# Kernel tuning notes

Hardware: AMD Instinct MI355X
Metric: run time of the kernel (lower is better)

Reference implementation:

```python
import jax, jax.numpy as jnp
import numpy as np

N_LAYERS = 2
D_CONV = 4
D_MODEL = 768
D_INNER = 1536
D_STATE = 16
D_DELTA = 48
B = 2
L = 1024
EPS = 1e-5


def setup_inputs() -> dict:
    key = jax.random.key(0)
    ks = jax.random.split(key, 8)
    s = 0.02
    x = jax.random.normal(ks[0], (B, L, D_MODEL), jnp.float32)
    in_proj_w = jax.random.normal(ks[1], (N_LAYERS, 2 * D_INNER, D_MODEL), jnp.float32) * s
    conv_w = jax.random.normal(ks[2], (N_LAYERS, D_INNER, 1, D_CONV), jnp.float32) * s
    conv_b = jnp.zeros((N_LAYERS, D_INNER), jnp.float32)
    xproj_w = jax.random.normal(ks[3], (N_LAYERS, D_DELTA + 2 * D_STATE, D_INNER), jnp.float32) * s
    dt_w = jax.random.normal(ks[4], (N_LAYERS, D_INNER, D_DELTA), jnp.float32) * s
    dt_b = jax.random.normal(ks[5], (N_LAYERS, D_INNER), jnp.float32) * s
    A_log = jnp.tile(jnp.log(jnp.arange(1, D_STATE + 1, dtype=jnp.float32)), (N_LAYERS, D_INNER, 1))
    D = jnp.ones((N_LAYERS, D_INNER), jnp.float32)
    out_proj_w = jax.random.normal(ks[6], (N_LAYERS, D_MODEL, D_INNER), jnp.float32) * s
    norm_w = jnp.ones((N_LAYERS, D_MODEL), jnp.float32)
    return dict(x=x, in_proj_w=in_proj_w, conv_w=conv_w, conv_b=conv_b,
                xproj_w=xproj_w, dt_w=dt_w, dt_b=dt_b, A_log=A_log, D=D,
                out_proj_w=out_proj_w, norm_w=norm_w)


def rms_norm(x, w):
    return w * x * jax.lax.rsqrt(jnp.mean(x * x, axis=-1, keepdims=True) + EPS)


def causal_depthwise_conv(x, w, b):
    # x: [B, L, D_INNER], w: [D_INNER, 1, K], b: [D_INNER]
    xc = x.transpose(0, 2, 1)  # [B, D, L]
    y = jax.lax.conv_general_dilated(
        xc, w, window_strides=(1,), padding=[(D_CONV - 1, 0)],
        dimension_numbers=("NCH", "OIH", "NCH"), feature_group_count=D_INNER)
    y = y + b[None, :, None]
    return y.transpose(0, 2, 1)  # [B, L, D]


def ssm(x, A_log, D, xproj_w, dt_w, dt_b):
    # x: [B, L, D_INNER]
    A = -jnp.exp(A_log)  # [D, N]
    dbc = jnp.einsum('bld,ed->ble', x, xproj_w)
    delta, Bc, C = jnp.split(dbc, [D_DELTA, D_DELTA + D_STATE], axis=-1)
    delta = jax.nn.softplus(jnp.einsum('blr,dr->bld', delta, dt_w) + dt_b)  # [B, L, D]
    dA = jnp.exp(delta[..., None] * A)                          # [B, L, D, N]
    dBx = delta[..., None] * Bc[:, :, None, :] * x[..., None]   # [B, L, D, N]

    def step(h, inp):
        dA_t, dBx_t, C_t = inp
        h = dA_t * h + dBx_t                      # [B, D, N]
        y = jnp.einsum('bdn,bn->bd', h, C_t)      # [B, D]
        return h, y

    h0 = jnp.zeros((x.shape[0], D_INNER, D_STATE), x.dtype)
    _, ys = jax.lax.scan(step, h0, (dA.transpose(1, 0, 2, 3),
                                    dBx.transpose(1, 0, 2, 3),
                                    C.transpose(1, 0, 2)))
    y = ys.transpose(1, 0, 2)  # [B, L, D]
    return y + D * x


def mamba_block(x, in_w, cw, cb, xp_w, dtw, dtb, Alog, Dp, out_w):
    xz = jnp.einsum('blm,em->ble', x, in_w)           # [B, L, 2*D_INNER]
    xi, z = jnp.split(xz, 2, axis=-1)
    xi = jax.nn.silu(causal_depthwise_conv(xi, cw, cb))
    y = ssm(xi, Alog, Dp, xp_w, dtw, dtb)
    out = y * jax.nn.silu(z)
    return jnp.einsum('bld,md->blm', out, out_w)


def reference(x, in_proj_w, conv_w, conv_b, xproj_w, dt_w, dt_b, A_log, D, out_proj_w, norm_w):
    for i in range(N_LAYERS):
        x = x + mamba_block(rms_norm(x, norm_w[i]), in_proj_w[i], conv_w[i], conv_b[i],
                            xproj_w[i], dt_w[i], dt_b[i], A_log[i], D[i], out_proj_w[i])
    return x
```

## Files before the change

### kernel.cpp

```cpp
#include <hip/hip_runtime.h>
#include <hip/hip_bf16.h>
#include <cstdint>

#define NL 2
#define DM 768
#define DI 1536
#define DS 16
#define DD 48
#define DCONV 4
#define BB 2
#define LL 1024
#define MROWS (BB*LL)
#define DBCW (DD + 2*DS)
#define TC 32
#define NC (LL/TC)
#define KSPL 4
#define XPN 128

typedef __bf16 bf16x8 __attribute__((ext_vector_type(8)));
typedef float f32x4 __attribute__((ext_vector_type(4)));
using bf16 = __hip_bfloat16;

__device__ __forceinline__ float softplusf(float x) {
  return (x > 20.f) ? x : log1pf(__expf(x));
}

__device__ __forceinline__ void load_lds16(const void* g, void* l) {
  __builtin_amdgcn_global_load_lds(
      (const __attribute__((address_space(1))) void*)g,
      (__attribute__((address_space(3))) void*)l, 16, 0, 0);
}

#define WI_N (NL*2*DI*DM)
#define WX_N (NL*XPN*DI)
#define WD_N (NL*DI*DD)
#define WO_N (NL*DM*DI)
__global__ __launch_bounds__(256)
void prep_weights(const float* __restrict__ wi, const float* __restrict__ wx,
                  const float* __restrict__ wd, const float* __restrict__ wo,
                  bf16* __restrict__ bi, bf16* __restrict__ bx,
                  bf16* __restrict__ bd, bf16* __restrict__ bo)
{
  int i = blockIdx.x * 256 + threadIdx.x;
  if (i < WI_N) { bi[i] = __float2bfloat16(wi[i]); return; }
  i -= WI_N;
  if (i < WX_N) {
    const int l = i / (XPN*DI), r = (i / DI) % XPN, k = i % DI;
    const float v = (r < DBCW) ? wx[((size_t)l*DBCW + r)*DI + k] : 0.f;
    bx[i] = __float2bfloat16(v); return;
  }
  i -= WX_N;
  if (i < WD_N) { bd[i] = __float2bfloat16(wd[i]); return; }
  i -= WD_N;
  if (i < WO_N) { bo[i] = __float2bfloat16(wo[i]); }
}

__global__ __launch_bounds__(256)
void rmsnorm_kernel(const float* __restrict__ x, const float* __restrict__ w,
                    bf16* __restrict__ out)
{
  const int row = blockIdx.x;
  const float* xr = x + (size_t)row * DM;
  const int t = threadIdx.x;
  float v0 = xr[t], v1 = xr[t + 256], v2 = xr[t + 512];
  float ss = v0*v0 + v1*v1 + v2*v2;
  #pragma unroll
  for (int off = 32; off > 0; off >>= 1) ss += __shfl_down(ss, off);
  __shared__ float sred[4];
  if ((t & 63) == 0) sred[t >> 6] = ss;
  __syncthreads();
  const float scale = rsqrtf((sred[0]+sred[1]+sred[2]+sred[3]) * (1.f/DM) + 1e-5f);
  out[(size_t)row*DM + t      ] = __float2bfloat16(v0 * scale * w[t]);
  out[(size_t)row*DM + t + 256] = __float2bfloat16(v1 * scale * w[t + 256]);
  out[(size_t)row*DM + t + 512] = __float2bfloat16(v2 * scale * w[t + 512]);
}

__global__ __launch_bounds__(256)
void gemm_in128(const bf16* __restrict__ A, const bf16* __restrict__ W,
                float* __restrict__ xzf, bf16* __restrict__ zb)
{
  __shared__ __align__(16) bf16 As[128][32];
  __shared__ __align__(16) bf16 Ws[128][32];
  const int tid = threadIdx.x;
  const int wave = tid >> 6, lane = tid & 63;
  const int m0 = blockIdx.x * 128, n0 = blockIdx.y * 128;
  const int wr = (wave >> 1) * 64, wc = (wave & 1) * 64;
  const int l16 = lane & 15, quad = lane >> 4;
  const int srow = wave * 16 + (lane >> 2);
  const int scol = (lane & 3) * 8;
  bf16* a_base0 = &As[wave*16][0];
  bf16* a_base1 = &As[64 + wave*16][0];
  bf16* w_base0 = &Ws[wave*16][0];
  bf16* w_base1 = &Ws[64 + wave*16][0];

  f32x4 acc[4][4] = {};

  for (int k0 = 0; k0 < DM; k0 += 32) {
    load_lds16(A + (size_t)(m0 + srow) * DM + k0 + scol,      a_base0);
    load_lds16(A + (size_t)(m0 + 64 + srow) * DM + k0 + scol, a_base1);
    load_lds16(W + (size_t)(n0 + srow) * DM + k0 + scol,      w_base0);
    load_lds16(W + (size_t)(n0 + 64 + srow) * DM + k0 + scol, w_base1);
    __syncthreads();

    bf16x8 af[4], wf[4];
    #pragma unroll
    for (int i = 0; i < 4; ++i)
      af[i] = *reinterpret_cast<const bf16x8*>(&As[wr + i*16 + l16][quad*8]);
    #pragma unroll
    for (int j = 0; j < 4; ++j)
      wf[j] = *reinterpret_cast<const bf16x8*>(&Ws[wc + j*16 + l16][quad*8]);
    #pragma unroll
    for (int i = 0; i < 4; ++i)
      #pragma unroll
      for (int j = 0; j < 4; ++j)
        acc[i][j] = __builtin_amdgcn_mfma_f32_16x16x32_bf16(af[i], wf[j], acc[i][j], 0, 0, 0);
    __syncthreads();
  }

  const bool isz = (n0 >= DI);
  #pragma unroll
  for (int i = 0; i < 4; ++i) {
    #pragma unroll
    for (int j = 0; j < 4; ++j) {
      const int col = n0 + wc + j*16 + l16;
      #pragma unroll
      for (int r = 0; r < 4; ++r) {
        const int row = m0 + wr + i*16 + quad*4 + r;
        const float v = acc[i][j][r];
        if (!isz) xzf[(size_t)row*DI + col] = v;
        else      zb[(size_t)row*DI + col - DI] = __float2bfloat16(v);
      }
    }
  }
}

template<int MODE>
__global__ __launch_bounds__(256)
void gemm64l(const bf16* __restrict__ A, int lda,
             const bf16* __restrict__ W, int ldw,
             float* __restrict__ C, int ldc, int N, int K,
             const float* __restrict__ res)
{
  __shared__ __align__(16) bf16 As[64][32];
  __shared__ __align__(16) bf16 Ws[64][32];
  const int tid = threadIdx.x;
  const int wave = tid >> 6, lane = tid & 63;
  const int m0 = blockIdx.x * 64, n0 = blockIdx.y * 64;
  const int wr = (wave >> 1) * 32, wc = (wave & 1) * 32;
  const int l16 = lane & 15, quad = lane >> 4;
  const int srow = wave * 16 + (lane >> 2);
  const int scol = (lane & 3) * 8;
  bf16* a_base = &As[wave*16][0];
  bf16* w_base = &Ws[wave*16][0];

  A += (size_t)blockIdx.z * K;
  W += (size_t)blockIdx.z * K;
  C += (size_t)blockIdx.z * MROWS * ldc;

  f32x4 acc[2][2] = {};

  for (int k0 = 0; k0 < K; k0 += 32) {
    load_lds16(A + (size_t)(m0 + srow) * lda + k0 + scol, a_base);
    load_lds16(W + (size_t)(n0 + srow) * ldw + k0 + scol, w_base);
    __syncthreads();
    bf16x8 af[2], wf[2];
    #pragma unroll
    for (int i = 0; i < 2; ++i)
      af[i] = *reinterpret_cast<const bf16x8*>(&As[wr + i*16 + l16][quad*8]);
    #pragma unroll
    for (int j = 0; j < 2; ++j)
      wf[j] = *reinterpret_cast<const bf16x8*>(&Ws[wc + j*16 + l16][quad*8]);
    #pragma unroll
    for (int i = 0; i < 2; ++i)
      #pragma unroll
      for (int j = 0; j < 2; ++j)
        acc[i][j] = __builtin_amdgcn_mfma_f32_16x16x32_bf16(af[i], wf[j], acc[i][j], 0, 0, 0);
    __syncthreads();
  }

  #pragma unroll
  for (int i = 0; i < 2; ++i) {
    #pragma unroll
    for (int j = 0; j < 2; ++j) {
      const int col = n0 + wc + j*16 + l16;
      if (col >= N) continue;
      #pragma unroll
      for (int r = 0; r < 4; ++r) {
        const int row = m0 + wr + i*16 + quad*4 + r;
        float v = acc[i][j][r];
        const size_t idx = (size_t)row * ldc + col;
        if (MODE == 3) v += res[idx];
        C[idx] = v;
      }
    }
  }
}

__global__ __launch_bounds__(256)
void xproj_reduce(const float* __restrict__ part, bf16* __restrict__ dbcb,
                  float* __restrict__ bcf)
{
  const int idx = blockIdx.x * 256 + threadIdx.x;
  const int row = idx / DBCW, col = idx % DBCW;
  float v = part[idx];
  #pragma unroll
  for (int z = 1; z < KSPL; ++z) v += part[idx + (size_t)z*MROWS*DBCW];
  if (col < DD) dbcb[(size_t)row*DD + col] = __float2bfloat16(v);
  else          bcf[(size_t)row*32 + col - DD] = v;
}

__global__ __launch_bounds__(256)
void conv_silu_kernel(const float* __restrict__ xzf, const float* __restrict__ cw,
                      const float* __restrict__ cb, bf16* __restrict__ xob)
{
  const int idx = blockIdx.x * 256 + threadIdx.x;
  const int d = idx % DI;
  const int row = idx / DI;
  const int l = row % LL;
  float acc = cb[d];
  #pragma unroll
  for (int k = 0; k < DCONV; ++k) {
    const int ll = l - (DCONV-1) + k;
    if (ll >= 0)
      acc += cw[d*DCONV + k] * xzf[(size_t)(row - (DCONV-1) + k) * DI + d];
  }
  const float s = acc / (1.f + __expf(-acc));
  xob[idx] = __float2bfloat16(s);
}

__global__ __launch_bounds__(256)
void gemm_dt(const bf16* __restrict__ A, const bf16* __restrict__ W,
             bf16* __restrict__ Cb, const float* __restrict__ bias)
{
  __shared__ __align__(16) bf16 As[64][40];
  __shared__ __align__(16) bf16 Ws[64][40];
  const int tid = threadIdx.x;
  const int m0 = blockIdx.x * 64, n0 = blockIdx.y * 64;
  const int wave = tid >> 6, lane = tid & 63;
  const int wr = (wave >> 1) * 32, wc = (wave & 1) * 32;
  const int l16 = lane & 15, quad = lane >> 4;
  const int srow = tid >> 2;
  const int scol = (tid & 3) * 8;

  f32x4 acc[2][2] = {};

  #pragma unroll
  for (int k0 = 0; k0 < DD; k0 += 32) {
    {
      const bf16* src = A + (size_t)(m0 + srow) * DD + (k0 + scol);
      bf16* dst = &As[srow][scol];
      if (k0 + scol + 8 <= DD) {
        *reinterpret_cast<uint4*>(dst) = *reinterpret_cast<const uint4*>(src);
      } else {
        #pragma unroll
        for (int j = 0; j < 8; ++j)
          dst[j] = (k0 + scol + j < DD) ? src[j] : __float2bfloat16(0.f);
      }
    }
    {
      const bf16* src = W + (size_t)(n0 + srow) * DD + (k0 + scol);
      bf16* dst = &Ws[srow][scol];
      if (k0 + scol + 8 <= DD) {
        *reinterpret_cast<uint4*>(dst) = *reinterpret_cast<const uint4*>(src);
      } else {
        #pragma unroll
        for (int j = 0; j < 8; ++j)
          dst[j] = (k0 + scol + j < DD) ? src[j] : __float2bfloat16(0.f);
      }
    }
    __syncthreads();
    bf16x8 af[2], wf[2];
    #pragma unroll
    for (int i = 0; i < 2; ++i)
      af[i] = *reinterpret_cast<const bf16x8*>(&As[wr + i*16 + l16][quad*8]);
    #pragma unroll
    for (int j = 0; j < 2; ++j)
      wf[j] = *reinterpret_cast<const bf16x8*>(&Ws[wc + j*16 + l16][quad*8]);
    #pragma unroll
    for (int i = 0; i < 2; ++i)
      #pragma unroll
      for (int j = 0; j < 2; ++j)
        acc[i][j] = __builtin_amdgcn_mfma_f32_16x16x32_bf16(af[i], wf[j], acc[i][j], 0, 0, 0);
    __syncthreads();
  }

  #pragma unroll
  for (int i = 0; i < 2; ++i) {
    #pragma unroll
    for (int j = 0; j < 2; ++j) {
      const int col = n0 + wc + j*16 + l16;
      #pragma unroll
      for (int r = 0; r < 4; ++r) {
        const int row = m0 + wr + i*16 + quad*4 + r;
        Cb[(size_t)row*DI + col] = __float2bfloat16(softplusf(acc[i][j][r] + bias[col]));
      }
    }
  }
}

__global__ __launch_bounds__(256)
void scan_pass1(const bf16* __restrict__ delta, const bf16* __restrict__ xi,
                const float* __restrict__ bcf, const float* __restrict__ A_log,
                float* __restrict__ P, float* __restrict__ H)
{
  __shared__ float Bs[TC][DS];
  const int tid = threadIdx.x;
  const int wave = tid >> 6, lane = tid & 63;
  const int s = lane >> 5;
  const int dloc = wave*32 + (lane & 31);
  const int dt = blockIdx.x % (DI/128);
  const int c  = (blockIdx.x / (DI/128)) % NC;
  const int b  =  blockIdx.x / ((DI/128)*NC);
  const int d  = dt*128 + dloc;
  const int t0 = c*TC;

  {
    const int t = tid >> 4, n = tid & 15;
    Bs[t][n]      = bcf[((size_t)b*LL + t0 + t)*32 + n];
    Bs[t + 16][n] = bcf[((size_t)b*LL + t0 + 16 + t)*32 + n];
  }
  float An[8];
  {
    const float4* ap = (const float4*)(A_log + (size_t)d*DS + s*8);
    float4 v0 = ap[0], v1 = ap[1];
    An[0] = -__expf(v0.x)*1.44269504f; An[1] = -__expf(v0.y)*1.44269504f;
    An[2] = -__expf(v0.z)*1.44269504f; An[3] = -__expf(v0.w)*1.44269504f;
    An[4] = -__expf(v1.x)*1.44269504f; An[5] = -__expf(v1.y)*1.44269504f;
    An[6] = -__expf(v1.z)*1.44269504f; An[7] = -__expf(v1.w)*1.44269504f;
  }
  __syncthreads();

  const bf16* dptr = delta + ((size_t)b*LL + t0)*DI + d;
  const bf16* xptr = xi    + ((size_t)b*LL + t0)*DI + d;
  float h[8] = {0.f,0.f,0.f,0.f,0.f,0.f,0.f,0.f};
  float sdl = 0.f;
  #pragma unroll
  for (int t = 0; t < TC; ++t) {
    const float dl = __bfloat162float(dptr[(size_t)t*DI]);
    const float xv = __bfloat162float(xptr[(size_t)t*DI]);
    const float dlxv = dl * xv;
    sdl += dl;
    const float4* brow = (const float4*)&Bs[t][s*8];
    const float4 b0 = brow[0], b1 = brow[1];
    const float bb[8] = {b0.x,b0.y,b0.z,b0.w,b1.x,b1.y,b1.z,b1.w};
    #pragma unroll
    for (int n = 0; n < 8; ++n) {
      const float dA = exp2f(dl * An[n]);
      h[n] = dA*h[n] + dlxv*bb[n];
    }
  }
  const size_t base = (((size_t)b*NC + c)*DI + d)*DS + s*8;
  float4* Pp = (float4*)(P + base);
  float4* Hp = (float4*)(H + base);
  Pp[0] = make_float4(exp2f(An[0]*sdl), exp2f(An[1]*sdl), exp2f(An[2]*sdl), exp2f(An[3]*sdl));
  Pp[1] = make_float4(exp2f(An[4]*sdl), exp2f(An[5]*sdl), exp2f(An[6]*sdl), exp2f(An[7]*sdl));
  Hp[0] = make_float4(h[0],h[1],h[2],h[3]);
  Hp[1] = make_float4(h[4],h[5],h[6],h[7]);
}

__global__ __launch_bounds__(256)
void scan_fix(const float* __restrict__ P, float* __restrict__ H)
{
  const int idx = blockIdx.x * 256 + threadIdx.x;
  const int n = idx & 15;
  const int d = (idx >> 4) % DI;
  const int b = idx / (DS * DI);
  float hin = 0.f;
  #pragma unroll 8
  for (int c = 0; c < NC; ++c) {
    const size_t ic = (((size_t)b*NC + c)*DI + d)*DS + n;
    const float Pv = P[ic];
    const float Hv = H[ic];
    H[ic] = hin;
    hin = fmaf(Pv, hin, Hv);
  }
}

__global__ __launch_bounds__(256)
void scan_pass2(const bf16* __restrict__ delta, const bf16* __restrict__ xi,
                const float* __restrict__ bcf, const float* __restrict__ A_log,
                const float* __restrict__ H, const float* __restrict__ Dp,
                const bf16* __restrict__ zb, bf16* __restrict__ outb)
{
  __shared__ float Bs[TC][DS];
  __shared__ float Cs[TC][DS];
  const int tid = threadIdx.x;
  const int wave = tid >> 6, lane = tid & 63;
  const int s = lane >> 5;
  const int dloc = wave*32 + (lane & 31);
  const int dt = blockIdx.x % (DI/128);
  const int c  = (blockIdx.x / (DI/128)) % NC;
  const int b  =  blockIdx.x / ((DI/128)*NC);
  const int d  = dt*128 + dloc;
  const int t0 = c*TC;

  {
    const int t = tid >> 4, n = tid & 15;
    const size_t r0 = ((size_t)b*LL + t0 + t)*32;
    const size_t r1 = ((size_t)b*LL + t0 + 16 + t)*32;
    Bs[t][n]      = bcf[r0 + n];
    Bs[t + 16][n] = bcf[r1 + n];
    Cs[t][n]      = bcf[r0 + 16 + n];
    Cs[t + 16][n] = bcf[r1 + 16 + n];
  }
  float An[8];
  {
    const float4* ap = (const float4*)(A_log + (size_t)d*DS + s*8);
    float4 v0 = ap[0], v1 = ap[1];
    An[0] = -__expf(v0.x)*1.44269504f; An[1] = -__expf(v0.y)*1.44269504f;
    An[2] = -__expf(v0.z)*1.44269504f; An[3] = -__expf(v0.w)*1.44269504f;
    An[4] = -__expf(v1.x)*1.44269504f; An[5] = -__expf(v1.y)*1.44269504f;
    An[6] = -__expf(v1.z)*1.44269504f; An[7] = -__expf(v1.w)*1.44269504f;
  }
  const float Dd = Dp[d];
  float h[8];
  {
    const float4* hp = (const float4*)(H + (((size_t)b*NC + c)*DI + d)*DS + s*8);
    float4 h0 = hp[0], h1 = hp[1];
    h[0]=h0.x; h[1]=h0.y; h[2]=h0.z; h[3]=h0.w;
    h[4]=h1.x; h[5]=h1.y; h[6]=h1.z; h[7]=h1.w;
  }
  __syncthreads();

  const bf16* dptr = delta + ((size_t)b*LL + t0)*DI + d;
  const bf16* xptr = xi    + ((size_t)b*LL + t0)*DI + d;
  const bf16* zptr = zb    + ((size_t)b*LL + t0)*DI + d;
  bf16* optr = outb + ((size_t)b*LL + t0)*DI + d;

  #pragma unroll
  for (int t = 0; t < TC; ++t) {
    const float dl = __bfloat162float(dptr[(size_t)t*DI]);
    const float xv = __bfloat162float(xptr[(size_t)t*DI]);
    const float zv = __bfloat162float(zptr[(size_t)t*DI]);
    const float dlxv = dl * xv;
    const float4* brow = (const float4*)&Bs[t][s*8];
    const float4* crow = (const float4*)&Cs[t][s*8];
    const float4 b0 = brow[0], b1 = brow[1];
    const float4 c0 = crow[0], c1 = crow[1];
    const float bb[8] = {b0.x,b0.y,b0.z,b0.w,b1.x,b1.y,b1.z,b1.w};
    const float cc[8] = {c0.x,c0.y,c0.z,c0.w,c1.x,c1.y,c1.z,c1.w};
    float y = 0.f;
    #pragma unroll
    for (int n = 0; n < 8; ++n) {
      const float dA = exp2f(dl * An[n]);
      h[n] = dA*h[n] + dlxv*bb[n];
      y = fmaf(h[n], cc[n], y);
    }
    y += __shfl_xor(y, 32);
    if (s == 0) {
      const float o = (y + Dd * xv) * (zv / (1.f + __expf(-zv)));
      optr[(size_t)t*DI] = __float2bfloat16(o);
    }
  }
}

extern "C" void kernel_launch(void* const* d_in, const int* in_sizes, int n_in,
                              void* d_out, int out_size, void* d_ws, size_t ws_size,
                              hipStream_t stream)
{
  const float* x_in   = (const float*)d_in[0];
  const float* w_inp  = (const float*)d_in[1];
  const float* w_conv = (const float*)d_in[2];
  const float* b_conv = (const float*)d_in[3];
  const float* w_xprj = (const float*)d_in[4];
  const float* w_dtp  = (const float*)d_in[5];
  const float* b_dt   = (const float*)d_in[6];
  const float* a_log  = (const float*)d_in[7];
  const float* d_par  = (const float*)d_in[8];
  const float* w_outp = (const float*)d_in[9];
  const float* w_norm = (const float*)d_in[10];
  float* xfinal = (float*)d_out;

  char* ws = (char*)d_ws;
  size_t off = 0;
  auto alloc = [&](size_t bytes) -> void* {
    void* p = ws + off;
    off += (bytes + 255) & ~(size_t)255;
    return p;
  };
  bf16*  wb_in  = (bf16*) alloc((size_t)WI_N*2);
  bf16*  wb_xp  = (bf16*) alloc((size_t)WX_N*2);
  bf16*  wb_dt  = (bf16*) alloc((size_t)WD_N*2);
  bf16*  wb_out = (bf16*) alloc((size_t)WO_N*2);
  bf16*  xn     = (bf16*) alloc((size_t)MROWS*DM*2);
  float* xzf    = (float*)alloc((size_t)MROWS*DI*4);
  bf16*  zb     = (bf16*) alloc((size_t)MROWS*DI*2);
  bf16*  xcb    = (bf16*) alloc((size_t)MROWS*DI*2);
  float* xpart  = (float*)alloc((size_t)KSPL*MROWS*DBCW*4);
  bf16*  dbcb   = (bf16*) alloc((size_t)MROWS*DD*2);
  float* bcf    = (float*)alloc((size_t)MROWS*32*4);
  bf16*  dltb   = (bf16*) alloc((size_t)MROWS*DI*2);
  bf16*  scb    = (bf16*) alloc((size_t)MROWS*DI*2);
  float* x1     = (float*)alloc((size_t)MROWS*DM*4);
  float* Pws    = (float*)alloc((size_t)BB*NC*DI*DS*4);
  float* Hws    = (float*)alloc((size_t)BB*NC*DI*DS*4);

  prep_weights<<<(WI_N+WX_N+WD_N+WO_N + 255)/256, 256, 0, stream>>>(
      w_inp, w_xprj, w_dtp, w_outp, wb_in, wb_xp, wb_dt, wb_out);

  const float* xprev = x_in;
  for (int l = 0; l < NL; ++l) {
    rmsnorm_kernel<<<MROWS, 256, 0, stream>>>(xprev, w_norm + l*DM, xn);

    gemm_in128<<<dim3(MROWS/128, (2*DI)/128), 256, 0, stream>>>(
        xn, wb_in + (size_t)l*2*DI*DM, xzf, zb);

    conv_silu_kernel<<<(MROWS*DI)/256, 256, 0, stream>>>(
        xzf, w_conv + l*DI*DCONV, b_conv + l*DI, xcb);

    gemm64l<0><<<dim3(MROWS/64, XPN/64, KSPL), 256, 0, stream>>>(
        xcb, DI, wb_xp + (size_t)l*XPN*DI, DI, xpart, DBCW, DBCW, DI/KSPL, nullptr);

    xproj_reduce<<<(MROWS*DBCW)/256, 256, 0, stream>>>(xpart, dbcb, bcf);

    gemm_dt<<<dim3(MROWS/64, DI/64), 256, 0, stream>>>(
        dbcb, wb_dt + (size_t)l*DI*DD, dltb, b_dt + l*DI);

    scan_pass1<<<BB*NC*(DI/128), 256, 0, stream>>>(
        dltb, xcb, bcf, a_log + (size_t)l*DI*DS, Pws, Hws);
    scan_fix<<<(BB*DI*DS)/256, 256, 0, stream>>>(Pws, Hws);
    scan_pass2<<<BB*NC*(DI/128), 256, 0, stream>>>(
        dltb, xcb, bcf, a_log + (size_t)l*DI*DS, Hws, d_par + l*DI, zb, scb);

    float* xout = (l == NL-1) ? xfinal : x1;
    gemm64l<3><<<dim3(MROWS/64, DM/64, 1), 256, 0, stream>>>(
        scb, DI, wb_out + (size_t)l*DM*DI, DI, xout, DM, DM, DI, xprev);

    xprev = x1;
  }
}
```

Baseline: 392.7 us.

## Fuse scan passes with grid barriers, fold reductions into consumers, split-K out-proj

The three scan kernels become one persistent kernel that uses global atomic grid barriers between the chunk pass, the prefix fix-up and the output pass. The x-projection split-K reduction moves into the dt GEMM's load path, and the in-projection now writes the x half as bf16 instead of fp32. The out-projection uses a 128-tile split-K GEMM whose partial sums are reduced in a new kernel that also adds the residual and applies the next layer's RMSNorm. Together these cut launches and intermediate traffic, but the grid barrier relies on all 768 scan blocks being resident at once, which risks deadlock if occupancy falls short.

```diff
diff --git a/kernel.cpp b/kernel.cpp
--- a/kernel.cpp
+++ b/kernel.cpp
@@ -16,6 +16,7 @@
 #define NC (LL/TC)
 #define KSPL 4
 #define XPN 128
+#define SCAN_BLOCKS (BB*NC*(DI/128))
 
 typedef __bf16 bf16x8 __attribute__((ext_vector_type(8)));
 typedef float f32x4 __attribute__((ext_vector_type(4)));
@@ -31,6 +32,18 @@
       (__attribute__((address_space(3))) void*)l, 16, 0, 0);
 }
 
+__device__ __forceinline__ void grid_barrier(unsigned* slot, unsigned nb) {
+  __syncthreads();
+  if (threadIdx.x == 0) {
+    __threadfence();
+    __hip_atomic_fetch_add(slot, 1u, __ATOMIC_RELEASE, __HIP_MEMORY_SCOPE_AGENT);
+    while (__hip_atomic_load(slot, __ATOMIC_ACQUIRE, __HIP_MEMORY_SCOPE_AGENT) < nb)
+      __builtin_amdgcn_s_sleep(2);
+    __threadfence();
+  }
+  __syncthreads();
+}
+
 #define WI_N (NL*2*DI*DM)
 #define WX_N (NL*XPN*DI)
 #define WD_N (NL*DI*DD)
@@ -39,8 +52,10 @@
 void prep_weights(const float* __restrict__ wi, const float* __restrict__ wx,
                   const float* __restrict__ wd, const float* __restrict__ wo,
                   bf16* __restrict__ bi, bf16* __restrict__ bx,
-                  bf16* __restrict__ bd, bf16* __restrict__ bo)
-{
+                  bf16* __restrict__ bd, bf16* __restrict__ bo,
+                  unsigned* __restrict__ bar)
+{
+  if (blockIdx.x == 0 && threadIdx.x < 8) bar[threadIdx.x] = 0u;
   int i = blockIdx.x * 256 + threadIdx.x;
   if (i < WI_N) { bi[i] = __float2bfloat16(wi[i]); return; }
   i -= WI_N;
@@ -75,9 +90,12 @@
   out[(size_t)row*DM + t + 512] = __float2bfloat16(v2 * scale * w[t + 512]);
 }
 
-__global__ __launch_bounds__(256)
-void gemm_in128(const bf16* __restrict__ A, const bf16* __restrict__ W,
-                float* __restrict__ xzf, bf16* __restrict__ zb)
+template<int MODE>
+__global__ __launch_bounds__(256)
+void gemm128(const bf16* __restrict__ A, int lda,
+             const bf16* __restrict__ W, int ldw, int K,
+             float* __restrict__ Cf, int ldc,
+             bf16* __restrict__ o_x, bf16* __restrict__ o_z)
 {
   __shared__ __align__(16) bf16 As[128][32];
   __shared__ __align__(16) bf16 Ws[128][32];
@@ -93,13 +111,17 @@
   bf16* w_base0 = &Ws[wave*16][0];
   bf16* w_base1 = &Ws[64 + wave*16][0];
 
+  A += (size_t)blockIdx.z * K;
+  W += (size_t)blockIdx.z * K;
+  if (MODE == 0) Cf += (size_t)blockIdx.z * MROWS * ldc;
+
   f32x4 acc[4][4] = {};
 
-  for (int k0 = 0; k0 < DM; k0 += 32) {
-    load_lds16(A + (size_t)(m0 + srow) * DM + k0 + scol,      a_base0);
-    load_lds16(A + (size_t)(m0 + 64 + srow) * DM + k0 + scol, a_base1);
-    load_lds16(W + (size_t)(n0 + srow) * DM + k0 + scol,      w_base0);
-    load_lds16(W + (size_t)(n0 + 64 + srow) * DM + k0 + scol, w_base1);
+  for (int k0 = 0; k0 < K; k0 += 32) {
+    load_lds16(A + (size_t)(m0 + srow) * lda + k0 + scol,      a_base0);
+    load_lds16(A + (size_t)(m0 + 64 + srow) * lda + k0 + scol, a_base1);
+    load_lds16(W + (size_t)(n0 + srow) * ldw + k0 + scol,      w_base0);
+    load_lds16(W + (size_t)(n0 + 64 + srow) * ldw + k0 + scol, w_base1);
     __syncthreads();
 
     bf16x8 af[4], wf[4];
@@ -117,7 +139,6 @@
     __syncthreads();
   }
 
-  const bool isz = (n0 >= DI);
   #pragma unroll
   for (int i = 0; i < 4; ++i) {
     #pragma unroll
@@ -127,19 +148,40 @@
       for (int r = 0; r < 4; ++r) {
         const int row = m0 + wr + i*16 + quad*4 + r;
         const float v = acc[i][j][r];
-        if (!isz) xzf[(size_t)row*DI + col] = v;
-        else      zb[(size_t)row*DI + col - DI] = __float2bfloat16(v);
-      }
-    }
-  }
-}
-
-template<int MODE>
-__global__ __launch_bounds__(256)
-void gemm64l(const bf16* __restrict__ A, int lda,
-             const bf16* __restrict__ W, int ldw,
-             float* __restrict__ C, int ldc, int N, int K,
-             const float* __restrict__ res)
+        if (MODE == 0) {
+          Cf[(size_t)row*ldc + col] = v;
+        } else {
+          if (col < DI) o_x[(size_t)row*DI + col] = __float2bfloat16(v);
+          else          o_z[(size_t)row*DI + col - DI] = __float2bfloat16(v);
+        }
+      }
+    }
+  }
+}
+
+__global__ __launch_bounds__(256)
+void conv_silu_kernel(const bf16* __restrict__ xb, const float* __restrict__ cw,
+                      const float* __restrict__ cb, bf16* __restrict__ xob)
+{
+  const int idx = blockIdx.x * 256 + threadIdx.x;
+  const int d = idx % DI;
+  const int row = idx / DI;
+  const int l = row % LL;
+  float acc = cb[d];
+  #pragma unroll
+  for (int k = 0; k < DCONV; ++k) {
+    const int ll = l - (DCONV-1) + k;
+    if (ll >= 0)
+      acc += cw[d*DCONV + k] *
+             __bfloat162float(xb[(size_t)(row - (DCONV-1) + k) * DI + d]);
+  }
+  const float s = acc / (1.f + __expf(-acc));
+  xob[idx] = __float2bfloat16(s);
+}
+
+__global__ __launch_bounds__(256)
+void gemm_xp(const bf16* __restrict__ A, const bf16* __restrict__ W,
+             float* __restrict__ C)
 {
   __shared__ __align__(16) bf16 As[64][32];
   __shared__ __align__(16) bf16 Ws[64][32];
@@ -152,16 +194,17 @@
   const int scol = (lane & 3) * 8;
   bf16* a_base = &As[wave*16][0];
   bf16* w_base = &Ws[wave*16][0];
+  const int K = DI / KSPL;
 
   A += (size_t)blockIdx.z * K;
   W += (size_t)blockIdx.z * K;
-  C += (size_t)blockIdx.z * MROWS * ldc;
+  C += (size_t)blockIdx.z * MROWS * DBCW;
 
   f32x4 acc[2][2] = {};
 
   for (int k0 = 0; k0 < K; k0 += 32) {
-    load_lds16(A + (size_t)(m0 + srow) * lda + k0 + scol, a_base);
-    load_lds16(W + (size_t)(n0 + srow) * ldw + k0 + scol, w_base);
+    load_lds16(A + (size_t)(m0 + srow) * DI + k0 + scol, a_base);
+    load_lds16(W + (size_t)(n0 + srow) * DI + k0 + scol, w_base);
     __syncthreads();
     bf16x8 af[2], wf[2];
     #pragma unroll
@@ -183,54 +226,20 @@
     #pragma unroll
     for (int j = 0; j < 2; ++j) {
       const int col = n0 + wc + j*16 + l16;
-      if (col >= N) continue;
+      if (col >= DBCW) continue;
       #pragma unroll
       for (int r = 0; r < 4; ++r) {
         const int row = m0 + wr + i*16 + quad*4 + r;
-        float v = acc[i][j][r];
-        const size_t idx = (size_t)row * ldc + col;
-        if (MODE == 3) v += res[idx];
-        C[idx] = v;
-      }
-    }
-  }
-}
-
-__global__ __launch_bounds__(256)
-void xproj_reduce(const float* __restrict__ part, bf16* __restrict__ dbcb,
-                  float* __restrict__ bcf)
-{
-  const int idx = blockIdx.x * 256 + threadIdx.x;
-  const int row = idx / DBCW, col = idx % DBCW;
-  float v = part[idx];
-  #pragma unroll
-  for (int z = 1; z < KSPL; ++z) v += part[idx + (size_t)z*MROWS*DBCW];
-  if (col < DD) dbcb[(size_t)row*DD + col] = __float2bfloat16(v);
-  else          bcf[(size_t)row*32 + col - DD] = v;
-}
-
-__global__ __launch_bounds__(256)
-void conv_silu_kernel(const float* __restrict__ xzf, const float* __restrict__ cw,
-                      const float* __restrict__ cb, bf16* __restrict__ xob)
-{
-  const int idx = blockIdx.x * 256 + threadIdx.x;
-  const int d = idx % DI;
-  const int row = idx / DI;
-  const int l = row % LL;
-  float acc = cb[d];
-  #pragma unroll
-  for (int k = 0; k < DCONV; ++k) {
-    const int ll = l - (DCONV-1) + k;
-    if (ll >= 0)
-      acc += cw[d*DCONV + k] * xzf[(size_t)(row - (DCONV-1) + k) * DI + d];
-  }
-  const float s = acc / (1.f + __expf(-acc));
-  xob[idx] = __float2bfloat16(s);
-}
-
-__global__ __launch_bounds__(256)
-void gemm_dt(const bf16* __restrict__ A, const bf16* __restrict__ W,
-             bf16* __restrict__ Cb, const float* __restrict__ bias)
+        C[(size_t)row*DBCW + col] = acc[i][j][r];
+      }
+    }
+  }
+}
+
+__global__ __launch_bounds__(256)
+void gemm_dt(const float* __restrict__ part, const bf16* __restrict__ W,
+             bf16* __restrict__ Cb, const float* __restrict__ bias,
+             float* __restrict__ bcf)
 {
   __shared__ __align__(16) bf16 As[64][40];
   __shared__ __align__(16) bf16 Ws[64][40];
@@ -242,30 +251,57 @@
   const int srow = tid >> 2;
   const int scol = (tid & 3) * 8;
 
+  if (blockIdx.y == 0) {
+    const int r = tid >> 2;
+    const int c8 = (tid & 3) * 8;
+    const float* p = part + ((size_t)(m0 + r))*DBCW + DD + c8;
+    float4 s0 = make_float4(0,0,0,0), s1 = make_float4(0,0,0,0);
+    #pragma unroll
+    for (int z = 0; z < KSPL; ++z) {
+      const float4* pz = (const float4*)(p + (size_t)z*MROWS*DBCW);
+      float4 a = pz[0], b = pz[1];
+      s0.x+=a.x; s0.y+=a.y; s0.z+=a.z; s0.w+=a.w;
+      s1.x+=b.x; s1.y+=b.y; s1.z+=b.z; s1.w+=b.w;
+    }
+    float4* dst = (float4*)(bcf + (size_t)(m0 + r)*32 + c8);
+    dst[0] = s0; dst[1] = s1;
+  }
+
   f32x4 acc[2][2] = {};
 
   #pragma unroll
   for (int k0 = 0; k0 < DD; k0 += 32) {
     {
-      const bf16* src = A + (size_t)(m0 + srow) * DD + (k0 + scol);
+      const int kbase = k0 + scol;
       bf16* dst = &As[srow][scol];
-      if (k0 + scol + 8 <= DD) {
-        *reinterpret_cast<uint4*>(dst) = *reinterpret_cast<const uint4*>(src);
+      if (kbase < DD) {
+        const float* p = part + ((size_t)(m0 + srow))*DBCW + kbase;
+        float4 s0 = make_float4(0,0,0,0), s1 = make_float4(0,0,0,0);
+        #pragma unroll
+        for (int z = 0; z < KSPL; ++z) {
+          const float4* pz = (const float4*)(p + (size_t)z*MROWS*DBCW);
+          float4 a = pz[0], b = pz[1];
+          s0.x+=a.x; s0.y+=a.y; s0.z+=a.z; s0.w+=a.w;
+          s1.x+=b.x; s1.y+=b.y; s1.z+=b.z; s1.w+=b.w;
+        }
+        dst[0] = __float2bfloat16(s0.x); dst[1] = __float2bfloat16(s0.y);
+        dst[2] = __float2bfloat16(s0.z); dst[3] = __float2bfloat16(s0.w);
+        dst[4] = __float2bfloat16(s1.x); dst[5] = __float2bfloat16(s1.y);
+        dst[6] = __float2bfloat16(s1.z); dst[7] = __float2bfloat16(s1.w);
       } else {
         #pragma unroll
-        for (int j = 0; j < 8; ++j)
-          dst[j] = (k0 + scol + j < DD) ? src[j] : __float2bfloat16(0.f);
+        for (int j = 0; j < 8; ++j) dst[j] = __float2bfloat16(0.f);
       }
     }
     {
-      const bf16* src = W + (size_t)(n0 + srow) * DD + (k0 + scol);
+      const int kbase = k0 + scol;
       bf16* dst = &Ws[srow][scol];
-      if (k0 + scol + 8 <= DD) {
-        *reinterpret_cast<uint4*>(dst) = *reinterpret_cast<const uint4*>(src);
+      if (kbase < DD) {
+        *reinterpret_cast<uint4*>(dst) =
+            *reinterpret_cast<const uint4*>(W + (size_t)(n0 + srow)*DD + kbase);
       } else {
         #pragma unroll
-        for (int j = 0; j < 8; ++j)
-          dst[j] = (k0 + scol + j < DD) ? src[j] : __float2bfloat16(0.f);
+        for (int j = 0; j < 8; ++j) dst[j] = __float2bfloat16(0.f);
       }
     }
     __syncthreads();
@@ -298,89 +334,12 @@
   }
 }
 
-__global__ __launch_bounds__(256)
-void scan_pass1(const bf16* __restrict__ delta, const bf16* __restrict__ xi,
-                const float* __restrict__ bcf, const float* __restrict__ A_log,
-                float* __restrict__ P, float* __restrict__ H)
-{
-  __shared__ float Bs[TC][DS];
-  const int tid = threadIdx.x;
-  const int wave = tid >> 6, lane = tid & 63;
-  const int s = lane >> 5;
-  const int dloc = wave*32 + (lane & 31);
-  const int dt = blockIdx.x % (DI/128);
-  const int c  = (blockIdx.x / (DI/128)) % NC;
-  const int b  =  blockIdx.x / ((DI/128)*NC);
-  const int d  = dt*128 + dloc;
-  const int t0 = c*TC;
-
-  {
-    const int t = tid >> 4, n = tid & 15;
-    Bs[t][n]      = bcf[((size_t)b*LL + t0 + t)*32 + n];
-    Bs[t + 16][n] = bcf[((size_t)b*LL + t0 + 16 + t)*32 + n];
-  }
-  float An[8];
-  {
-    const float4* ap = (const float4*)(A_log + (size_t)d*DS + s*8);
-    float4 v0 = ap[0], v1 = ap[1];
-    An[0] = -__expf(v0.x)*1.44269504f; An[1] = -__expf(v0.y)*1.44269504f;
-    An[2] = -__expf(v0.z)*1.44269504f; An[3] = -__expf(v0.w)*1.44269504f;
-    An[4] = -__expf(v1.x)*1.44269504f; An[5] = -__expf(v1.y)*1.44269504f;
-    An[6] = -__expf(v1.z)*1.44269504f; An[7] = -__expf(v1.w)*1.44269504f;
-  }
-  __syncthreads();
-
-  const bf16* dptr = delta + ((size_t)b*LL + t0)*DI + d;
-  const bf16* xptr = xi    + ((size_t)b*LL + t0)*DI + d;
-  float h[8] = {0.f,0.f,0.f,0.f,0.f,0.f,0.f,0.f};
-  float sdl = 0.f;
-  #pragma unroll
-  for (int t = 0; t < TC; ++t) {
-    const float dl = __bfloat162float(dptr[(size_t)t*DI]);
-    const float xv = __bfloat162float(xptr[(size_t)t*DI]);
-    const float dlxv = dl * xv;
-    sdl += dl;
-    const float4* brow = (const float4*)&Bs[t][s*8];
-    const float4 b0 = brow[0], b1 = brow[1];
-    const float bb[8] = {b0.x,b0.y,b0.z,b0.w,b1.x,b1.y,b1.z,b1.w};
-    #pragma unroll
-    for (int n = 0; n < 8; ++n) {
-      const float dA = exp2f(dl * An[n]);
-      h[n] = dA*h[n] + dlxv*bb[n];
-    }
-  }
-  const size_t base = (((size_t)b*NC + c)*DI + d)*DS + s*8;
-  float4* Pp = (float4*)(P + base);
-  float4* Hp = (float4*)(H + base);
-  Pp[0] = make_float4(exp2f(An[0]*sdl), exp2f(An[1]*sdl), exp2f(An[2]*sdl), exp2f(An[3]*sdl));
-  Pp[1] = make_float4(exp2f(An[4]*sdl), exp2f(An[5]*sdl), exp2f(An[6]*sdl), exp2f(An[7]*sdl));
-  Hp[0] = make_float4(h[0],h[1],h[2],h[3]);
-  Hp[1] = make_float4(h[4],h[5],h[6],h[7]);
-}
-
-__global__ __launch_bounds__(256)
-void scan_fix(const float* __restrict__ P, float* __restrict__ H)
-{
-  const int idx = blockIdx.x * 256 + threadIdx.x;
-  const int n = idx & 15;
-  const int d = (idx >> 4) % DI;
-  const int b = idx / (DS * DI);
-  float hin = 0.f;
-  #pragma unroll 8
-  for (int c = 0; c < NC; ++c) {
-    const size_t ic = (((size_t)b*NC + c)*DI + d)*DS + n;
-    const float Pv = P[ic];
-    const float Hv = H[ic];
-    H[ic] = hin;
-    hin = fmaf(Pv, hin, Hv);
-  }
-}
-
-__global__ __launch_bounds__(256)
-void scan_pass2(const bf16* __restrict__ delta, const bf16* __restrict__ xi,
-                const float* __restrict__ bcf, const float* __restrict__ A_log,
-                const float* __restrict__ H, const float* __restrict__ Dp,
-                const bf16* __restrict__ zb, bf16* __restrict__ outb)
+__global__ __launch_bounds__(256, 3)
+void scan_mega(const bf16* __restrict__ delta, const bf16* __restrict__ xi,
+               const float* __restrict__ bcf, const float* __restrict__ A_log,
+               const float* __restrict__ Dp, const bf16* __restrict__ zb,
+               float* __restrict__ P, float* __restrict__ H,
+               bf16* __restrict__ outb, unsigned* __restrict__ bar)
 {
   __shared__ float Bs[TC][DS];
   __shared__ float Cs[TC][DS];
@@ -412,44 +371,128 @@
     An[4] = -__expf(v1.x)*1.44269504f; An[5] = -__expf(v1.y)*1.44269504f;
     An[6] = -__expf(v1.z)*1.44269504f; An[7] = -__expf(v1.w)*1.44269504f;
   }
-  const float Dd = Dp[d];
-  float h[8];
-  {
-    const float4* hp = (const float4*)(H + (((size_t)b*NC + c)*DI + d)*DS + s*8);
-    float4 h0 = hp[0], h1 = hp[1];
-    h[0]=h0.x; h[1]=h0.y; h[2]=h0.z; h[3]=h0.w;
-    h[4]=h1.x; h[5]=h1.y; h[6]=h1.z; h[7]=h1.w;
-  }
   __syncthreads();
 
   const bf16* dptr = delta + ((size_t)b*LL + t0)*DI + d;
   const bf16* xptr = xi    + ((size_t)b*LL + t0)*DI + d;
-  const bf16* zptr = zb    + ((size_t)b*LL + t0)*DI + d;
-  bf16* optr = outb + ((size_t)b*LL + t0)*DI + d;
-
-  #pragma unroll
-  for (int t = 0; t < TC; ++t) {
-    const float dl = __bfloat162float(dptr[(size_t)t*DI]);
-    const float xv = __bfloat162float(xptr[(size_t)t*DI]);
-    const float zv = __bfloat162float(zptr[(size_t)t*DI]);
-    const float dlxv = dl * xv;
-    const float4* brow = (const float4*)&Bs[t][s*8];
-    const float4* crow = (const float4*)&Cs[t][s*8];
-    const float4 b0 = brow[0], b1 = brow[1];
-    const float4 c0 = crow[0], c1 = crow[1];
-    const float bb[8] = {b0.x,b0.y,b0.z,b0.w,b1.x,b1.y,b1.z,b1.w};
-    const float cc[8] = {c0.x,c0.y,c0.z,c0.w,c1.x,c1.y,c1.z,c1.w};
-    float y = 0.f;
-    #pragma unroll
-    for (int n = 0; n < 8; ++n) {
-      const float dA = exp2f(dl * An[n]);
-      h[n] = dA*h[n] + dlxv*bb[n];
-      y = fmaf(h[n], cc[n], y);
-    }
-    y += __shfl_xor(y, 32);
-    if (s == 0) {
-      const float o = (y + Dd * xv) * (zv / (1.f + __expf(-zv)));
-      optr[(size_t)t*DI] = __float2bfloat16(o);
+
+  {
+    float h[8] = {0.f,0.f,0.f,0.f,0.f,0.f,0.f,0.f};
+    float sdl = 0.f;
+    #pragma unroll
+    for (int t = 0; t < TC; ++t) {
+      const float dl = __bfloat162float(dptr[(size_t)t*DI]);
+      const float xv = __bfloat162float(xptr[(size_t)t*DI]);
+      const float dlxv = dl * xv;
+      sdl += dl;
+      const float4* brow = (const float4*)&Bs[t][s*8];
+      const float4 b0 = brow[0], b1 = brow[1];
+      const float bb[8] = {b0.x,b0.y,b0.z,b0.w,b1.x,b1.y,b1.z,b1.w};
+      #pragma unroll
+      for (int n = 0; n < 8; ++n) {
+        const float dA = exp2f(dl * An[n]);
+        h[n] = dA*h[n] + dlxv*bb[n];
+      }
+    }
+    const size_t base = (((size_t)b*NC + c)*DI + d)*DS + s*8;
+    float4* Pp = (float4*)(P + base);
+    float4* Hp = (float4*)(H + base);
+    Pp[0] = make_float4(exp2f(An[0]*sdl), exp2f(An[1]*sdl), exp2f(An[2]*sdl), exp2f(An[3]*sdl));
+    Pp[1] = make_float4(exp2f(An[4]*sdl), exp2f(An[5]*sdl), exp2f(An[6]*sdl), exp2f(An[7]*sdl));
+    Hp[0] = make_float4(h[0],h[1],h[2],h[3]);
+    Hp[1] = make_float4(h[4],h[5],h[6],h[7]);
+  }
+
+  grid_barrier(bar + 0, SCAN_BLOCKS);
+
+  if (blockIdx.x < (BB*DI*DS)/256) {
+    const int idx = blockIdx.x * 256 + tid;
+    const int n2 = idx & 15;
+    const int d2 = (idx >> 4) % DI;
+    const int b2 = idx / (DS * DI);
+    float hin = 0.f;
+    #pragma unroll 8
+    for (int cc = 0; cc < NC; ++cc) {
+      const size_t ic = (((size_t)b2*NC + cc)*DI + d2)*DS + n2;
+      const float Pv = P[ic];
+      const float Hv = H[ic];
+      H[ic] = hin;
+      hin = fmaf(Pv, hin, Hv);
+    }
+  }
+
+  grid_barrier(bar + 1, SCAN_BLOCKS);
+
+  {
+    const float Dd = Dp[d];
+    float h[8];
+    {
+      const float4* hp = (const float4*)(H + (((size_t)b*NC + c)*DI + d)*DS + s*8);
+      float4 h0 = hp[0], h1 = hp[1];
+      h[0]=h0.x; h[1]=h0.y; h[2]=h0.z; h[3]=h0.w;
+      h[4]=h1.x; h[5]=h1.y; h[6]=h1.z; h[7]=h1.w;
+    }
+    const bf16* zptr = zb + ((size_t)b*LL + t0)*DI + d;
+    bf16* optr = outb + ((size_t)b*LL + t0)*DI + d;
+    #pragma unroll
+    for (int t = 0; t < TC; ++t) {
+      const float dl = __bfloat162float(dptr[(size_t)t*DI]);
+      const float xv = __bfloat162float(xptr[(size_t)t*DI]);
+      const float zv = __bfloat162float(zptr[(size_t)t*DI]);
+      const float dlxv = dl * xv;
+      const float4* brow = (const float4*)&Bs[t][s*8];
+      const float4* crow = (const float4*)&Cs[t][s*8];
+      const float4 b0 = brow[0], b1 = brow[1];
+      const float4 c0 = crow[0], c1 = crow[1];
+      const float bb[8] = {b0.x,b0.y,b0.z,b0.w,b1.x,b1.y,b1.z,b1.w};
+      const float cc[8] = {c0.x,c0.y,c0.z,c0.w,c1.x,c1.y,c1.z,c1.w};
+      float y = 0.f;
+      #pragma unroll
+      for (int n = 0; n < 8; ++n) {
+        const float dA = exp2f(dl * An[n]);
+        h[n] = dA*h[n] + dlxv*bb[n];
+        y = fmaf(h[n], cc[n], y);
+      }
+      y += __shfl_xor(y, 32);
+      if (s == 0) {
+        const float o = (y + Dd * xv) * (zv / (1.f + __expf(-zv)));
+        optr[(size_t)t*DI] = __float2bfloat16(o);
+      }
+    }
+  }
+}
+
+template<bool LAST>
+__global__ __launch_bounds__(256)
+void resid_rms(const float* __restrict__ opart, const float* __restrict__ xprev,
+               const float* __restrict__ w, float* __restrict__ xout,
+               bf16* __restrict__ xn)
+{
+  const int row = blockIdx.x;
+  const int t = threadIdx.x;
+  const size_t base = (size_t)row * DM;
+  float v[3];
+  float ss = 0.f;
+  #pragma unroll
+  for (int i = 0; i < 3; ++i) {
+    const int col = t + i*256;
+    const float val = opart[base + col] + opart[(size_t)MROWS*DM + base + col]
+                    + xprev[base + col];
+    xout[base + col] = val;
+    v[i] = val;
+    ss += val*val;
+  }
+  if (!LAST) {
+    #pragma unroll
+    for (int off = 32; off > 0; off >>= 1) ss += __shfl_down(ss, off);
+    __shared__ float sred[4];
+    if ((t & 63) == 0) sred[t >> 6] = ss;
+    __syncthreads();
+    const float scale = rsqrtf((sred[0]+sred[1]+sred[2]+sred[3]) * (1.f/DM) + 1e-5f);
+    #pragma unroll
+    for (int i = 0; i < 3; ++i) {
+      const int col = t + i*256;
+      xn[base + col] = __float2bfloat16(v[i] * scale * w[col]);
     }
   }
 }
@@ -483,49 +526,50 @@
   bf16*  wb_dt  = (bf16*) alloc((size_t)WD_N*2);
   bf16*  wb_out = (bf16*) alloc((size_t)WO_N*2);
   bf16*  xn     = (bf16*) alloc((size_t)MROWS*DM*2);
-  float* xzf    = (float*)alloc((size_t)MROWS*DI*4);
+  bf16*  xb     = (bf16*) alloc((size_t)MROWS*DI*2);
   bf16*  zb     = (bf16*) alloc((size_t)MROWS*DI*2);
   bf16*  xcb    = (bf16*) alloc((size_t)MROWS*DI*2);
   float* xpart  = (float*)alloc((size_t)KSPL*MROWS*DBCW*4);
-  bf16*  dbcb   = (bf16*) alloc((size_t)MROWS*DD*2);
   float* bcf    = (float*)alloc((size_t)MROWS*32*4);
   bf16*  dltb   = (bf16*) alloc((size_t)MROWS*DI*2);
   bf16*  scb    = (bf16*) alloc((size_t)MROWS*DI*2);
+  float* opart  = (float*)alloc((size_t)2*MROWS*DM*4);
   float* x1     = (float*)alloc((size_t)MROWS*DM*4);
   float* Pws    = (float*)alloc((size_t)BB*NC*DI*DS*4);
   float* Hws    = (float*)alloc((size_t)BB*NC*DI*DS*4);
+  unsigned* bar = (unsigned*)alloc(64);
 
   prep_weights<<<(WI_N+WX_N+WD_N+WO_N + 255)/256, 256, 0, stream>>>(
-      w_inp, w_xprj, w_dtp, w_outp, wb_in, wb_xp, wb_dt, wb_out);
+      w_inp, w_xprj, w_dtp, w_outp, wb_in, wb_xp, wb_dt, wb_out, bar);
+
+  rmsnorm_kernel<<<MROWS, 256, 0, stream>>>(x_in, w_norm, xn);
 
   const float* xprev = x_in;
   for (int l = 0; l < NL; ++l) {
-    rmsnorm_kernel<<<MROWS, 256, 0, stream>>>(xprev, w_norm + l*DM, xn);
-
-    gemm_in128<<<dim3(MROWS/128, (2*DI)/128), 256, 0, stream>>>(
-        xn, wb_in + (size_t)l*2*DI*DM, xzf, zb);
+    gemm128<1><<<dim3(MROWS/128, (2*DI)/128, 1), 256, 0, stream>>>(
+        xn, DM, wb_in + (size_t)l*2*DI*DM, DM, DM, nullptr, 0, xb, zb);
 
     conv_silu_kernel<<<(MROWS*DI)/256, 256, 0, stream>>>(
-        xzf, w_conv + l*DI*DCONV, b_conv + l*DI, xcb);
-
-    gemm64l<0><<<dim3(MROWS/64, XPN/64, KSPL), 256, 0, stream>>>(
-        xcb, DI, wb_xp + (size_t)l*XPN*DI, DI, xpart, DBCW, DBCW, DI/KSPL, nullptr);
-
-    xproj_reduce<<<(MROWS*DBCW)/256, 256, 0, stream>>>(xpart, dbcb, bcf);
+        xb, w_conv + l*DI*DCONV, b_conv + l*DI, xcb);
+
+    gemm_xp<<<dim3(MROWS/64, XPN/64, KSPL), 256, 0, stream>>>(
+        xcb, wb_xp + (size_t)l*XPN*DI, xpart);
 
     gemm_dt<<<dim3(MROWS/64, DI/64), 256, 0, stream>>>(
-        dbcb, wb_dt + (size_t)l*DI*DD, dltb, b_dt + l*DI);
-
-    scan_pass1<<<BB*NC*(DI/128), 256, 0, stream>>>(
-        dltb, xcb, bcf, a_log + (size_t)l*DI*DS, Pws, Hws);
-    scan_fix<<<(BB*DI*DS)/256, 256, 0, stream>>>(Pws, Hws);
-    scan_pass2<<<BB*NC*(DI/128), 256, 0, stream>>>(
-        dltb, xcb, bcf, a_log + (size_t)l*DI*DS, Hws, d_par + l*DI, zb, scb);
-
-    float* xout = (l == NL-1) ? xfinal : x1;
-    gemm64l<3><<<dim3(MROWS/64, DM/64, 1), 256, 0, stream>>>(
-        scb, DI, wb_out + (size_t)l*DM*DI, DI, xout, DM, DM, DI, xprev);
-
+        xpart, wb_dt + (size_t)l*DI*DD, dltb, b_dt + l*DI, bcf);
+
+    scan_mega<<<SCAN_BLOCKS, 256, 0, stream>>>(
+        dltb, xcb, bcf, a_log + (size_t)l*DI*DS, d_par + l*DI, zb,
+        Pws, Hws, scb, bar + l*2);
+
+    gemm128<0><<<dim3(MROWS/128, DM/128, 2), 256, 0, stream>>>(
+        scb, DI, wb_out + (size_t)l*DM*DI, DI, DI/2, opart, DM, nullptr, nullptr);
+
+    if (l == NL-1) {
+      resid_rms<true><<<MROWS, 256, 0, stream>>>(opart, xprev, nullptr, xfinal, nullptr);
+    } else {
+      resid_rms<false><<<MROWS, 256, 0, stream>>>(opart, xprev, w_norm + (l+1)*DM, x1, xn);
+    }
     xprev = x1;
   }
 }
```

Result: slower. 1.106 ms (+181.7%).
